# Performance work log

Hardware: AMD Instinct MI355X
Metric: run time of the kernel (lower is better)

Reference implementation:

```python
import jax, jax.numpy as jnp
import numpy as np

EMBED_DIM = 1024
HEAD_DIM = 64
B, S = 4, 4096


def setup_inputs() -> dict:
    key = jax.random.key(0)
    ks = jax.random.split(key, 9)
    scale = 1.0 / np.sqrt(EMBED_DIM)
    return {
        "Q": jax.random.normal(ks[0], (B, S, EMBED_DIM), jnp.float32),
        "K": jax.random.normal(ks[1], (B, S, EMBED_DIM), jnp.float32),
        "V": jax.random.normal(ks[2], (B, S, EMBED_DIM), jnp.float32),
        "mask": jnp.ones((1, S, S), jnp.int32),
        "Wq": jax.random.normal(ks[3], (EMBED_DIM, HEAD_DIM), jnp.float32) * scale,
        "bq": jax.random.normal(ks[4], (HEAD_DIM,), jnp.float32) * scale,
        "Wk": jax.random.normal(ks[5], (EMBED_DIM, HEAD_DIM), jnp.float32) * scale,
        "bk": jax.random.normal(ks[6], (HEAD_DIM,), jnp.float32) * scale,
        "Wv": jax.random.normal(ks[7], (EMBED_DIM, HEAD_DIM), jnp.float32) * scale,
        "bv": jax.random.normal(ks[8], (HEAD_DIM,), jnp.float32) * scale,
    }


def reference(Q, K, V, mask, Wq, bq, Wk, bk, Wv, bv):
    # Per-head projections: [B,S,E] @ [E,D] -> [B,S,D]
    q = Q @ Wq + bq
    k = K @ Wk + bk
    v = V @ Wv + bv
    d_k = q.shape[-1]
    # scores: [B,Sq,Sk]
    scores = jnp.einsum("bqd,bkd->bqk", q, k) / jnp.sqrt(jnp.float32(d_k))
    scores = jnp.where(mask == 0, -jnp.inf, scores)
    p_attn = jax.nn.softmax(scores, axis=-1)
    return jnp.einsum("bqk,bkd->bqd", p_attn, v)
```

## Files before the change

### kernel.cpp

```cpp
#include <hip/hip_runtime.h>

#define B_ 4
#define S_ 4096
#define E_ 1024
#define D_ 64

typedef __attribute__((ext_vector_type(8))) short short8;
typedef __attribute__((ext_vector_type(4))) float floatx4;
typedef __attribute__((ext_vector_type(4))) unsigned int uint4v;

__device__ __forceinline__ floatx4 mfma_bf16(short8 a, short8 b, floatx4 c) {
    return __builtin_amdgcn_mfma_f32_16x16x32_bf16(a, b, c, 0, 0, 0);
}

__device__ __forceinline__ short f2bf(float f) {
    unsigned u = __builtin_bit_cast(unsigned, f);
    u = (u + 0x7FFFu + ((u >> 16) & 1u)) >> 16;
    return (short)u;
}

__device__ __forceinline__ unsigned pk2bf(float a, float b) {
    unsigned ua = __builtin_bit_cast(unsigned, a);
    unsigned ub = __builtin_bit_cast(unsigned, b);
    ua = (ua + 0x7FFFu + ((ua >> 16) & 1u)) >> 16;
    ub = (ub + 0x7FFFu + ((ub >> 16) & 1u)) & 0xFFFF0000u;
    return ua | ub;
}

__global__ __launch_bounds__(256) void prep_kernel(
    const float* __restrict__ Wq, const float* __restrict__ Wk, const float* __restrict__ Wv,
    short* __restrict__ WT, int* __restrict__ flag)
{
    int tid = blockIdx.x * 256 + threadIdx.x;
    if (tid == 0) *flag = 0;
    int mat = tid >> 16;
    int rem = tid & 65535;
    const float* W = (mat == 0) ? Wq : ((mat == 1) ? Wk : Wv);
    int n = rem >> 10, k = rem & 1023;
    WT[mat * 65536 + n * E_ + k] = f2bf(W[k * D_ + n]);
}

__global__ __launch_bounds__(256, 4) void proj_kernel(
    const float* __restrict__ Qm, const float* __restrict__ Km, const float* __restrict__ Vm,
    const short* __restrict__ WT,
    const float* __restrict__ bq, const float* __restrict__ bk, const float* __restrict__ bv,
    short* __restrict__ qs, short* __restrict__ ks, short* __restrict__ vT,
    const int4* __restrict__ mask4, int* __restrict__ flag)
{
    __shared__ __align__(16) float of[32 * 68];

    const int mat = blockIdx.y;
    const int bx  = blockIdx.x;
    const int tid = threadIdx.x;
    const int wv = tid >> 6, lane = tid & 63;
    const int quad = lane >> 4, c16 = lane & 15;
    const int rt = wv & 1, kh = wv >> 1;
    const int m0 = bx * 32 + rt * 16;

    const float* X    = (mat == 0) ? Qm : ((mat == 1) ? Km : Vm);
    const float* bias = (mat == 0) ? bq : ((mat == 1) ? bk : bv);
    const short* Wt   = WT + mat * 65536;

    const float* arow = X + (size_t)(m0 + c16) * E_ + kh * 512 + quad * 8;
    const short* wbase = Wt + (size_t)c16 * E_ + kh * 512 + quad * 8;

    floatx4 acc[4];
    #pragma unroll
    for (int f = 0; f < 4; ++f) acc[f] = (floatx4){0.f, 0.f, 0.f, 0.f};

    #pragma unroll 4
    for (int it = 0; it < 16; ++it) {
        float4 fa = *(const float4*)(arow + it * 32);
        float4 fb = *(const float4*)(arow + it * 32 + 4);
        uint4v uv;
        uv[0] = pk2bf(fa.x, fa.y); uv[1] = pk2bf(fa.z, fa.w);
        uv[2] = pk2bf(fb.x, fb.y); uv[3] = pk2bf(fb.z, fb.w);
        short8 a = __builtin_bit_cast(short8, uv);
        #pragma unroll
        for (int f = 0; f < 4; ++f) {
            short8 b = *(const short8*)(wbase + (size_t)f * 16384 + it * 32);
            acc[f] = mfma_bf16(a, b, acc[f]);
        }
    }

    if (kh == 1) {
        #pragma unroll
        for (int f = 0; f < 4; ++f)
            #pragma unroll
            for (int r = 0; r < 4; ++r)
                of[(rt * 16 + quad * 4 + r) * 68 + f * 16 + c16] = acc[f][r];
    }
    __syncthreads();
    if (kh == 0) {
        const float scale = (mat == 0) ? (0.125f * 1.4426950408889634f) : 1.0f;
        #pragma unroll
        for (int f = 0; f < 4; ++f) {
            float bb = bias[f * 16 + c16];
            #pragma unroll
            for (int r = 0; r < 4; ++r) {
                int m = m0 + quad * 4 + r;
                float v = (acc[f][r] + of[(rt * 16 + quad * 4 + r) * 68 + f * 16 + c16] + bb) * scale;
                short h = f2bf(v);
                if (mat == 0)      qs[(size_t)m * D_ + f * 16 + c16] = h;
                else if (mat == 1) ks[(size_t)m * D_ + f * 16 + c16] = h;
                else vT[((size_t)((m >> 12) * D_ + f * 16 + c16)) * S_ + (m & (S_ - 1))] = h;
            }
        }
    }

    {
        int btid = (mat * 512 + bx) * 256 + tid;
        const int stride = 1536 * 256;
        int found = 0;
        for (int i = btid; i < (S_ * S_ / 4); i += stride) {
            int4 v = mask4[i];
            found |= (v.x == 0) | (v.y == 0) | (v.z == 0) | (v.w == 0);
        }
        if (found) atomicOr(flag, 1);
    }
}

__global__ __launch_bounds__(512, 2) void flash_kernel(
    const short* __restrict__ qs, const short* __restrict__ ks,
    const short* __restrict__ vT, const int* __restrict__ mask,
    const int* __restrict__ flag, float* __restrict__ out)
{
    __shared__ __align__(16) char smem[47104];
    short* kst = (short*)smem;
    short* pst = kst + 18432;

    const int bid = blockIdx.x;
    const int b  = (bid & 7) >> 1;
    const int qt = ((bid >> 3) << 1) | (bid & 1);
    const int tid = threadIdx.x;
    const int w = tid >> 6;
    const int qw = w & 1, kwq = w >> 1;
    const int lane = tid & 63;
    const int quad = lane >> 4, c16 = lane & 15;
    const int m0 = qt * 32 + qw * 16;

    const short* qrow = qs + (size_t)(b * S_ + m0 + c16) * D_ + quad * 8;
    short8 aq0 = *(const short8*)(qrow);
    short8 aq1 = *(const short8*)(qrow + 32);

    const short* kbase = ks + (size_t)b * S_ * D_;
    const short* vbase = vT + (size_t)b * D_ * S_ + kwq * 1024;

    const int sq   = w >> 1;
    const int srow = (w & 1) * 16 + (lane >> 3);
    const int schunk = lane & 7;
    const short* gstage = kbase + ((size_t)sq * 1024 + srow) * D_ + schunk * 8;
    short* lstage = kst + sq * 2304 + srow * 72 + schunk * 8;

    floatx4 O[4];
    #pragma unroll
    for (int f = 0; f < 4; ++f) O[f] = (floatx4){0.f, 0.f, 0.f, 0.f};
    float lsum = 0.f;

    const int anyz = *flag;
    short* pw = pst + w * 640;
    short8 g0 = *(const short8*)(gstage);
    short8 g1 = *(const short8*)(gstage + 8 * D_);

    for (int kt = 0; kt < 32; ++kt) {
        const int buf = kt & 1;
        *(short8*)(lstage + buf * 9216)           = g0;
        *(short8*)(lstage + buf * 9216 + 8 * 72)  = g1;
        short8 gn0 = g0, gn1 = g1;
        if (kt < 31) {
            gn0 = *(const short8*)(gstage + (size_t)(kt + 1) * 2048);
            gn1 = *(const short8*)(gstage + (size_t)(kt + 1) * 2048 + 8 * D_);
        }
        __syncthreads();

        const int key0 = kt * 32;

        short8 vv[4];
        #pragma unroll
        for (int f = 0; f < 4; ++f)
            vv[f] = *(const short8*)(vbase + (size_t)(f * 16 + c16) * S_ + key0 + quad * 8);

        const short* kt_lds = kst + buf * 9216 + kwq * 2304;

        floatx4 s[2];
        #pragma unroll
        for (int f = 0; f < 2; ++f) {
            const short* krow = kt_lds + (f * 16 + c16) * 72 + quad * 8;
            short8 ka0 = *(const short8*)(krow);
            short8 ka1 = *(const short8*)(krow + 32);
            floatx4 t = (floatx4){0.f, 0.f, 0.f, 0.f};
            t = mfma_bf16(ka0, aq0, t);
            t = mfma_bf16(ka1, aq1, t);
            s[f] = t;
        }

        if (anyz) {
            #pragma unroll
            for (int f = 0; f < 2; ++f)
                #pragma unroll
                for (int r = 0; r < 4; ++r)
                    if (mask[(size_t)(m0 + c16) * S_ +
                             kwq * 1024 + key0 + f * 16 + quad * 4 + r] == 0)
                        s[f][r] = -__builtin_inff();
        }

        #pragma unroll
        for (int f = 0; f < 2; ++f) {
            float p0 = exp2f(s[f][0]), p1 = exp2f(s[f][1]);
            float p2 = exp2f(s[f][2]), p3 = exp2f(s[f][3]);
            lsum += (p0 + p1) + (p2 + p3);
            int2 pk = make_int2((int)pk2bf(p0, p1), (int)pk2bf(p2, p3));
            *(int2*)(pw + c16 * 40 + f * 16 + quad * 4) = pk;
        }

        short8 pa = *(const short8*)(pw + c16 * 40 + quad * 8);

        #pragma unroll
        for (int f = 0; f < 4; ++f) O[f] = mfma_bf16(pa, vv[f], O[f]);
        g0 = gn0; g1 = gn1;
    }

    lsum += __shfl_xor(lsum, 16);
    lsum += __shfl_xor(lsum, 32);

    __syncthreads();
    float* of = (float*)smem;
    float* lw = (float*)(smem + 34816);
    #pragma unroll
    for (int f = 0; f < 4; ++f)
        #pragma unroll
        for (int r = 0; r < 4; ++r)
            of[(kwq * 32 + qw * 16 + quad * 4 + r) * 68 + f * 16 + c16] = O[f][r];
    if (quad == 0) lw[kwq * 32 + qw * 16 + c16] = lsum;
    __syncthreads();

    {
        const int q = tid >> 4;
        const int col0 = (tid & 15) * 4;
        const float inv = 1.0f / (lw[q] + lw[32 + q] + lw[64 + q] + lw[96 + q]);
        float4 o = *(const float4*)&of[q * 68 + col0];
        #pragma unroll
        for (int k = 1; k < 4; ++k) {
            float4 t = *(const float4*)&of[(k * 32 + q) * 68 + col0];
            o.x += t.x; o.y += t.y; o.z += t.z; o.w += t.w;
        }
        o.x *= inv; o.y *= inv; o.z *= inv; o.w *= inv;
        *(float4*)(out + ((size_t)(b * S_ + qt * 32 + q)) * 64 + col0) = o;
    }
}

extern "C" void kernel_launch(void* const* d_in, const int* in_sizes, int n_in,
                              void* d_out, int out_size, void* d_ws, size_t ws_size,
                              hipStream_t stream)
{
    const float* Q   = (const float*)d_in[0];
    const float* K   = (const float*)d_in[1];
    const float* V   = (const float*)d_in[2];
    const int*  mask = (const int*) d_in[3];
    const float* Wq  = (const float*)d_in[4];
    const float* bq  = (const float*)d_in[5];
    const float* Wk  = (const float*)d_in[6];
    const float* bk  = (const float*)d_in[7];
    const float* Wv  = (const float*)d_in[8];
    const float* bv  = (const float*)d_in[9];
    float* out = (float*)d_out;

    short* qs = (short*)d_ws;
    short* ks = qs + (size_t)B_ * S_ * D_;
    short* vT = ks + (size_t)B_ * S_ * D_;
    short* WT = vT + (size_t)B_ * S_ * D_;
    int* flag = (int*)(WT + 3 * D_ * E_);

    prep_kernel<<<768, 256, 0, stream>>>(Wq, Wk, Wv, WT, flag);
    proj_kernel<<<dim3(512, 3), 256, 0, stream>>>(Q, K, V, WT, bq, bk, bv,
                                                  qs, ks, vT, (const int4*)mask, flag);
    flash_kernel<<<512, 512, 0, stream>>>(qs, ks, vT, mask, flag, out);
}
```

Measured before the change: 345.3 us.

## Stage projection inputs via direct global-to-LDS loads and retile V layout

The projection kernel now streams fp32 activation rows into a swizzled per-wave LDS buffer using global_load_lds, with weights double-buffered in registers, in place of direct per-lane global float4 loads. V's transposed output is written in a fragment-tiled layout so the flash kernel reads contiguous per-lane short8 chunks. Occupancy of the projection kernel drops (64KB LDS, launch bounds 2), which may reduce latency hiding.

```diff
diff --git a/kernel.cpp b/kernel.cpp
--- a/kernel.cpp
+++ b/kernel.cpp
@@ -25,6 +25,12 @@
     ua = (ua + 0x7FFFu + ((ua >> 16) & 1u)) >> 16;
     ub = (ub + 0x7FFFu + ((ub >> 16) & 1u)) & 0xFFFF0000u;
     return ua | ub;
+}
+
+__device__ __forceinline__ void gload_lds16(const void* g, void* l) {
+    __builtin_amdgcn_global_load_lds(
+        (const __attribute__((address_space(1))) void*)g,
+        (__attribute__((address_space(3))) void*)l, 16, 0, 0);
 }
 
 __global__ __launch_bounds__(256) void prep_kernel(
@@ -40,14 +46,15 @@
     WT[mat * 65536 + n * E_ + k] = f2bf(W[k * D_ + n]);
 }
 
-__global__ __launch_bounds__(256, 4) void proj_kernel(
+__global__ __launch_bounds__(256, 2) void proj_kernel(
     const float* __restrict__ Qm, const float* __restrict__ Km, const float* __restrict__ Vm,
     const short* __restrict__ WT,
     const float* __restrict__ bq, const float* __restrict__ bk, const float* __restrict__ bv,
     short* __restrict__ qs, short* __restrict__ ks, short* __restrict__ vT,
     const int4* __restrict__ mask4, int* __restrict__ flag)
 {
-    __shared__ __align__(16) float of[32 * 68];
+    __shared__ __align__(16) char smem[65536];
+    float* of = (float*)(smem + 32768);
 
     const int mat = blockIdx.y;
     const int bx  = blockIdx.x;
@@ -59,30 +66,68 @@
 
     const float* X    = (mat == 0) ? Qm : ((mat == 1) ? Km : Vm);
     const float* bias = (mat == 0) ? bq : ((mat == 1) ? bk : bv);
-    const short* Wt   = WT + mat * 65536;
-
-    const float* arow = X + (size_t)(m0 + c16) * E_ + kh * 512 + quad * 8;
-    const short* wbase = Wt + (size_t)c16 * E_ + kh * 512 + quad * 8;
+    const char*  Xp   = (const char*)X;
+
+    char* wlds = smem + wv * 16384;
+
+    #define ASTAGE(c_) do {                                              \
+        const size_t koff_ = (size_t)kh * 2048 + (size_t)(c_) * 1024;    \
+        _Pragma("unroll")                                                \
+        for (int i_ = 0; i_ < 16; ++i_) {                                \
+            gload_lds16(Xp + (size_t)(m0 + i_) * 4096 + koff_            \
+                           + (size_t)((lane ^ (i_ & 7)) << 4),           \
+                        wlds + i_ * 1024);                               \
+        }                                                                \
+    } while (0)
+
+    const short* wk = WT + mat * 65536 + (size_t)c16 * 1024 + quad * 8 + kh * 512;
+    #define WLOADM(n_, dst_) do {                                        \
+        _Pragma("unroll")                                                \
+        for (int f_ = 0; f_ < 4; ++f_)                                   \
+            dst_[f_] = *(const short8*)(wk + (n_) * 32 + f_ * 16384);    \
+    } while (0)
 
     floatx4 acc[4];
     #pragma unroll
     for (int f = 0; f < 4; ++f) acc[f] = (floatx4){0.f, 0.f, 0.f, 0.f};
-
-    #pragma unroll 4
-    for (int it = 0; it < 16; ++it) {
-        float4 fa = *(const float4*)(arow + it * 32);
-        float4 fb = *(const float4*)(arow + it * 32 + 4);
-        uint4v uv;
-        uv[0] = pk2bf(fa.x, fa.y); uv[1] = pk2bf(fa.z, fa.w);
-        uv[2] = pk2bf(fb.x, fb.y); uv[3] = pk2bf(fb.z, fb.w);
-        short8 a = __builtin_bit_cast(short8, uv);
-        #pragma unroll
-        for (int f = 0; f < 4; ++f) {
-            short8 b = *(const short8*)(wbase + (size_t)f * 16384 + it * 32);
-            acc[f] = mfma_bf16(a, b, acc[f]);
-        }
-    }
-
+    short8 wA[4], wB[4];
+
+    const char* ardA = wlds + c16 * 1024 + (size_t)(((2 * quad)     ^ (c16 & 7)) << 4);
+    const char* ardB = wlds + c16 * 1024 + (size_t)(((2 * quad + 1) ^ (c16 & 7)) << 4);
+
+    #define ASTEP(s_, n_, W_) do {                                       \
+        float4 fa_ = *(const float4*)(ardA + (s_) * 128);                \
+        float4 fb_ = *(const float4*)(ardB + (s_) * 128);                \
+        uint4v uv_;                                                      \
+        uv_[0] = pk2bf(fa_.x, fa_.y); uv_[1] = pk2bf(fa_.z, fa_.w);      \
+        uv_[2] = pk2bf(fb_.x, fb_.y); uv_[3] = pk2bf(fb_.z, fb_.w);      \
+        short8 a_ = __builtin_bit_cast(short8, uv_);                     \
+        _Pragma("unroll")                                                \
+        for (int f_ = 0; f_ < 4; ++f_)                                   \
+            acc[f_] = mfma_bf16(a_, W_[f_], acc[f_]);                    \
+        if ((n_) + 2 < 16) WLOADM((n_) + 2, W_);                         \
+    } while (0)
+
+    WLOADM(0, wA);
+    ASTAGE(0);
+    WLOADM(1, wB);
+    asm volatile("s_waitcnt vmcnt(0)" ::: "memory");
+
+    ASTEP(0, 0, wA); ASTEP(1, 1, wB); ASTEP(2, 2, wA); ASTEP(3, 3, wB);
+    ASTEP(4, 4, wA); ASTEP(5, 5, wB); ASTEP(6, 6, wA); ASTEP(7, 7, wB);
+
+    asm volatile("s_waitcnt lgkmcnt(0)" ::: "memory");
+    ASTAGE(1);
+    asm volatile("s_waitcnt vmcnt(0)" ::: "memory");
+
+    ASTEP(0,  8, wA); ASTEP(1,  9, wB); ASTEP(2, 10, wA); ASTEP(3, 11, wB);
+    ASTEP(4, 12, wA); ASTEP(5, 13, wB); ASTEP(6, 14, wA); ASTEP(7, 15, wB);
+
+    #undef ASTAGE
+    #undef WLOADM
+    #undef ASTEP
+
+    __syncthreads();
     if (kh == 1) {
         #pragma unroll
         for (int f = 0; f < 4; ++f)
@@ -96,14 +141,24 @@
         #pragma unroll
         for (int f = 0; f < 4; ++f) {
             float bb = bias[f * 16 + c16];
-            #pragma unroll
-            for (int r = 0; r < 4; ++r) {
-                int m = m0 + quad * 4 + r;
-                float v = (acc[f][r] + of[(rt * 16 + quad * 4 + r) * 68 + f * 16 + c16] + bb) * scale;
-                short h = f2bf(v);
-                if (mat == 0)      qs[(size_t)m * D_ + f * 16 + c16] = h;
-                else if (mat == 1) ks[(size_t)m * D_ + f * 16 + c16] = h;
-                else vT[((size_t)((m >> 12) * D_ + f * 16 + c16)) * S_ + (m & (S_ - 1))] = h;
+            if (mat == 2) {
+                float v0 = acc[0 + f][0] + of[(rt * 16 + quad * 4 + 0) * 68 + f * 16 + c16] + bb;
+                float v1 = acc[f][1] + of[(rt * 16 + quad * 4 + 1) * 68 + f * 16 + c16] + bb;
+                float v2 = acc[f][2] + of[(rt * 16 + quad * 4 + 2) * 68 + f * 16 + c16] + bb;
+                float v3 = acc[f][3] + of[(rt * 16 + quad * 4 + 3) * 68 + f * 16 + c16] + bb;
+                int2 pk = make_int2((int)pk2bf(v0, v1), (int)pk2bf(v2, v3));
+                const int lane2 = (rt * 2 + (quad >> 1)) * 16 + c16;
+                const int j0 = (quad & 1) * 4;
+                *(int2*)(vT + ((size_t)(bx * 4 + f) * 512 + lane2 * 8 + j0)) = pk;
+            } else {
+                #pragma unroll
+                for (int r = 0; r < 4; ++r) {
+                    int m = m0 + quad * 4 + r;
+                    float v = (acc[f][r] + of[(rt * 16 + quad * 4 + r) * 68 + f * 16 + c16] + bb) * scale;
+                    short h = f2bf(v);
+                    if (mat == 0) qs[(size_t)m * D_ + f * 16 + c16] = h;
+                    else          ks[(size_t)m * D_ + f * 16 + c16] = h;
+                }
             }
         }
     }
@@ -144,7 +199,7 @@
     short8 aq1 = *(const short8*)(qrow + 32);
 
     const short* kbase = ks + (size_t)b * S_ * D_;
-    const short* vbase = vT + (size_t)b * D_ * S_ + kwq * 1024;
+    const short* vbase = vT + (size_t)b * 262144 + (size_t)kwq * 65536;
 
     const int sq   = w >> 1;
     const int srow = (w & 1) * 16 + (lane >> 3);
@@ -178,7 +233,7 @@
         short8 vv[4];
         #pragma unroll
         for (int f = 0; f < 4; ++f)
-            vv[f] = *(const short8*)(vbase + (size_t)(f * 16 + c16) * S_ + key0 + quad * 8);
+            vv[f] = *(const short8*)(vbase + (size_t)kt * 2048 + f * 512 + lane * 8);
 
         const short* kt_lds = kst + buf * 9216 + kwq * 2304;
 
```

New measurement: 307.8 us. 10.9% less time.
